# Kernel tuning notes

Measured on AMD Instinct MI355X. Metric: run time of the kernel, lower is better.

The kernel has to match this reference:

```python
import jax, jax.numpy as jnp
import numpy as np

N_NODES = 50000
N_EDGES = 800000
D = 128  # d_feat == hidden_channels


def setup_inputs() -> dict:
    key = jax.random.key(0)
    ks = jax.random.split(key, 7)
    s = 1.0 / np.sqrt(D)
    return {
        "x": jax.random.normal(ks[0], (N_NODES, D), dtype=jnp.float32),
        "edge_index": jax.random.randint(ks[1], (2, N_EDGES), 0, N_NODES, dtype=jnp.int64),
        "W1_l": jax.random.normal(ks[2], (D, D), dtype=jnp.float32) * s,
        "b1": jnp.zeros((D,), dtype=jnp.float32),
        "W1_r": jax.random.normal(ks[3], (D, D), dtype=jnp.float32) * s,
        "W2_l": jax.random.normal(ks[4], (D, D), dtype=jnp.float32) * s,
        "b2": jnp.zeros((D,), dtype=jnp.float32),
        "W2_r": jax.random.normal(ks[5], (D, D), dtype=jnp.float32) * s,
    }


def reference(x, edge_index, W1_l, b1, W1_r, W2_l, b2, W2_r):
    src = edge_index[0]
    dst = edge_index[1]
    n = x.shape[0]
    # in-degree for mean aggregation (zero-degree nodes get 0 aggregate)
    deg = jax.ops.segment_sum(jnp.ones_like(src, dtype=x.dtype), dst, num_segments=n)
    inv_deg = (1.0 / jnp.maximum(deg, 1.0))[:, None]  # [N,1]

    def sage_conv(h, Wl, b, Wr):
        # mean over incoming neighbor messages, then lin_l(agg) + lin_r(h)
        agg = jax.ops.segment_sum(h[src], dst, num_segments=n) * inv_deg  # [N,D]
        return agg @ Wl + b + h @ Wr

    h = jax.nn.relu(sage_conv(x, W1_l, b1, W1_r))
    return sage_conv(h, W2_l, b2, W2_r)
```

## Files before the change

kernel.cpp:

```cpp
#include <hip/hip_runtime.h>
#include <hip/hip_bf16.h>

typedef __attribute__((ext_vector_type(8))) short bf16x8;
typedef __attribute__((ext_vector_type(4))) float f32x4;

#define CAP 64
#define SH  8

static __device__ inline unsigned short f2b(float f) {
    unsigned u = __float_as_uint(f);
    unsigned r = (u + 0x7FFFu + ((u >> 16) & 1u)) >> 16;
    return (unsigned short)r;
}
static __device__ inline float blo(unsigned u) { return __uint_as_float(u << 16); }
static __device__ inline float bhi(unsigned u) { return __uint_as_float(u & 0xFFFF0000u); }

__global__ void zero_kernel(int* __restrict__ p, int n) {
    int i = blockIdx.x * blockDim.x + threadIdx.x;
    if (i < n) p[i] = 0;
}

__global__ __launch_bounds__(256) void fill_shard_kernel(
        const int* __restrict__ ei, int* __restrict__ cursor,
        unsigned short* __restrict__ edge16, int E, int N, int G, int npg) {
    int s = blockIdx.x & (SH - 1);
    int i = blockIdx.x >> 3;
    int d_lo = s * npg;
    int d_hi = d_lo + npg; if (d_hi > N) d_hi = N;
    int C = (E + G - 1) / G;
    int e0 = i * C;
    int e1 = e0 + C; if (e1 > E) e1 = E;
    for (int e = e0 + threadIdx.x; e < e1; e += 256) {
        int d = ei[E + e];
        if (d < d_lo || d >= d_hi) continue;
        int src = ei[e];
        if ((unsigned)src >= (unsigned)N) src = 0;
        int pos = atomicAdd(&cursor[d], 1);
        if (pos < CAP) edge16[(size_t)d * CAP + pos] = (unsigned short)src;
    }
}

__global__ __launch_bounds__(256) void x2b_kernel(const float* __restrict__ x,
                                                  unsigned short* __restrict__ xb,
                                                  int n4) {
    int i = blockIdx.x * blockDim.x + threadIdx.x;
    if (i >= n4) return;
    float4 v = ((const float4*)x)[i];
    ushort4 b;
    b.x = f2b(v.x); b.y = f2b(v.y); b.z = f2b(v.z); b.w = f2b(v.w);
    ((ushort4*)xb)[i] = b;
}

__global__ __launch_bounds__(256) void aggregate_kernel(
        const unsigned short* __restrict__ in, const int* __restrict__ cursor,
        const unsigned short* __restrict__ edge16, const int* __restrict__ ei,
        unsigned short* __restrict__ agg, int E, int N) {
    int node = blockIdx.x * 4 + (threadIdx.x >> 6);
    if (node >= N) return;
    int lane = threadIdx.x & 63;
    int g = lane >> 4;
    int f = lane & 15;
    int deg = cursor[node];

    float acc[8];
    #pragma unroll
    for (int i = 0; i < 8; ++i) acc[i] = 0.f;

    if (deg <= CAP) {
        const unsigned short* base = edge16 + (size_t)node * CAP;
        int idx = (lane < deg) ? (int)base[lane] : 0;
        #pragma unroll 4
        for (int j = 0; j < deg; j += 4) {
            int e = j + g;
            int s = __shfl(idx, e & 63);
            if (e < deg) {
                uint4 v = *(const uint4*)(in + (size_t)s * 128 + f * 8);
                acc[0] += blo(v.x); acc[1] += bhi(v.x);
                acc[2] += blo(v.y); acc[3] += bhi(v.y);
                acc[4] += blo(v.z); acc[5] += bhi(v.z);
                acc[6] += blo(v.w); acc[7] += bhi(v.w);
            }
        }
    } else {
        for (int j = 0; j < E; j += 4) {
            int e = j + g;
            bool act = (e < E) && (ei[E + e] == node);
            if (act) {
                int s = ei[e];
                if ((unsigned)s >= (unsigned)N) s = 0;
                uint4 v = *(const uint4*)(in + (size_t)s * 128 + f * 8);
                acc[0] += blo(v.x); acc[1] += bhi(v.x);
                acc[2] += blo(v.y); acc[3] += bhi(v.y);
                acc[4] += blo(v.z); acc[5] += bhi(v.z);
                acc[6] += blo(v.w); acc[7] += bhi(v.w);
            }
        }
    }

    #pragma unroll
    for (int d = 16; d <= 32; d <<= 1) {
        #pragma unroll
        for (int i = 0; i < 8; ++i) acc[i] += __shfl_xor(acc[i], d);
    }

    if (g == 0) {
        float inv = 1.0f / (float)(deg > 1 ? deg : 1);
        uint4 o;
        o.x = (unsigned)f2b(acc[0] * inv) | ((unsigned)f2b(acc[1] * inv) << 16);
        o.y = (unsigned)f2b(acc[2] * inv) | ((unsigned)f2b(acc[3] * inv) << 16);
        o.z = (unsigned)f2b(acc[4] * inv) | ((unsigned)f2b(acc[5] * inv) << 16);
        o.w = (unsigned)f2b(acc[6] * inv) | ((unsigned)f2b(acc[7] * inv) << 16);
        *(uint4*)(agg + (size_t)node * 128 + f * 8) = o;
    }
}

__global__ void prep_w_kernel(const float* __restrict__ W1l, const float* __restrict__ W1r,
                              const float* __restrict__ W2l, const float* __restrict__ W2r,
                              unsigned short* __restrict__ wt) {
    int n = blockIdx.x & 127;
    int layer = blockIdx.x >> 7;
    int k = threadIdx.x;
    const float* Wlp = layer ? W2l : W1l;
    const float* Wrp = layer ? W2r : W1r;
    unsigned short* dst = wt + (size_t)layer * 128 * 256 + (size_t)n * 256;
    dst[k]       = f2b(Wlp[(size_t)k * 128 + n]);
    dst[k + 128] = f2b(Wrp[(size_t)k * 128 + n]);
}

template<int RELU, int OUT_BF16>
__global__ __launch_bounds__(256) void gemm_mfma_kernel(
        const unsigned short* __restrict__ Arow, const unsigned short* __restrict__ Xrow,
        const unsigned short* __restrict__ Wt, const float* __restrict__ bias,
        void* __restrict__ outp, int n) {
    constexpr int LDK = 264;
    __shared__ unsigned short sA[64 * LDK];
    int tid = threadIdx.x;
    int row0 = blockIdx.x * 64;

    #pragma unroll
    for (int it = 0; it < 8; ++it) {
        int c = tid + it * 256;
        int r = c >> 5;
        int q = c & 31;
        int row = row0 + r; if (row >= n) row = n - 1;
        uint4 v = (q < 16) ? ((const uint4*)(Arow + (size_t)row * 128))[q]
                           : ((const uint4*)(Xrow + (size_t)row * 128))[q - 16];
        *(uint4*)&sA[r * LDK + q * 8] = v;
    }
    __syncthreads();

    int lane = tid & 63;
    int wave = tid >> 6;
    int quad = lane >> 4;
    int tm   = lane & 15;

    f32x4 acc[4][2];
    #pragma unroll
    for (int m = 0; m < 4; ++m)
        #pragma unroll
        for (int j = 0; j < 2; ++j)
            acc[m][j] = (f32x4){0.f, 0.f, 0.f, 0.f};

    const unsigned short* wb0 = Wt + (size_t)(wave * 32 + tm) * 256;

    #pragma unroll
    for (int ks = 0; ks < 8; ++ks) {
        int k0 = ks * 32 + quad * 8;
        bf16x8 a[4], b[2];
        #pragma unroll
        for (int m = 0; m < 4; ++m)
            a[m] = *(const bf16x8*)&sA[(m * 16 + tm) * LDK + k0];
        #pragma unroll
        for (int j = 0; j < 2; ++j)
            b[j] = *(const bf16x8*)(wb0 + (size_t)j * 16 * 256 + k0);
        #pragma unroll
        for (int m = 0; m < 4; ++m)
            #pragma unroll
            for (int j = 0; j < 2; ++j)
                acc[m][j] = __builtin_amdgcn_mfma_f32_16x16x32_bf16(a[m], b[j], acc[m][j], 0, 0, 0);
    }

    #pragma unroll
    for (int j = 0; j < 2; ++j) {
        int ncol = wave * 32 + j * 16 + tm;
        float bb = bias[ncol];
        #pragma unroll
        for (int m = 0; m < 4; ++m) {
            #pragma unroll
            for (int reg = 0; reg < 4; ++reg) {
                int row = row0 + m * 16 + quad * 4 + reg;
                if (row >= n) continue;
                float v = acc[m][j][reg] + bb;
                if (RELU) v = v > 0.f ? v : 0.f;
                if (OUT_BF16)
                    ((unsigned short*)outp)[(size_t)row * 128 + ncol] = f2b(v);
                else
                    ((float*)outp)[(size_t)row * 128 + ncol] = v;
            }
        }
    }
}

extern "C" void kernel_launch(void* const* d_in, const int* in_sizes, int n_in,
                              void* d_out, int out_size, void* d_ws, size_t ws_size,
                              hipStream_t stream) {
    const float* x   = (const float*)d_in[0];
    const int*   ei  = (const int*)d_in[1];
    const float* W1l = (const float*)d_in[2];
    const float* b1  = (const float*)d_in[3];
    const float* W1r = (const float*)d_in[4];
    const float* W2l = (const float*)d_in[5];
    const float* b2  = (const float*)d_in[6];
    const float* W2r = (const float*)d_in[7];
    float* out = (float*)d_out;

    const int D = 128;
    const int N = in_sizes[0] / D;
    const int E = in_sizes[1] / 2;

    char* ws = (char*)d_ws;
    size_t off = 0;
    auto alloc = [&](size_t bytes) {
        size_t o = off;
        off = (off + bytes + 511) & ~(size_t)511;
        return (void*)(ws + o);
    };
    int*            cursor  = (int*)           alloc((size_t)N * 4);
    unsigned short* edge16  = (unsigned short*)alloc((size_t)N * CAP * 2);
    unsigned short* agg_bf  = (unsigned short*)alloc((size_t)N * D * 2);
    unsigned short* xb      = (unsigned short*)alloc((size_t)N * D * 2);
    unsigned short* wt      = (unsigned short*)alloc((size_t)2 * 128 * 256 * 2);
    unsigned short* h_bf = xb;
    (void)ws_size; (void)n_in; (void)out_size;

    zero_kernel<<<(N + 255) / 256, 256, 0, stream>>>(cursor, N);
    {
        int G = 256;
        int npg = (N + SH - 1) / SH;
        fill_shard_kernel<<<SH * G, 256, 0, stream>>>(ei, cursor, edge16, E, N, G, npg);
    }

    int n4 = N * D / 4;
    x2b_kernel<<<(n4 + 255) / 256, 256, 0, stream>>>(x, xb, n4);
    prep_w_kernel<<<256, 128, 0, stream>>>(W1l, W1r, W2l, W2r, wt);
    const unsigned short* wt1 = wt;
    const unsigned short* wt2 = wt + (size_t)128 * 256;

    int agg_grid  = (N + 3) / 4;
    int gemm_grid = (N + 63) / 64;

    aggregate_kernel<<<agg_grid, 256, 0, stream>>>(xb, cursor, edge16, ei, agg_bf, E, N);
    gemm_mfma_kernel<1, 1><<<gemm_grid, 256, 0, stream>>>(agg_bf, xb, wt1, b1, (void*)h_bf, N);

    aggregate_kernel<<<agg_grid, 256, 0, stream>>>(h_bf, cursor, edge16, ei, agg_bf, E, N);
    gemm_mfma_kernel<0, 0><<<gemm_grid, 256, 0, stream>>>(agg_bf, h_bf, wt2, b2, (void*)out, N);
}
```

Baseline: 229.8 us.

## Fuse neighbor aggregation into the MFMA GEMM kernel per layer

```diff
diff --git a/kernel.cpp b/kernel.cpp
--- a/kernel.cpp
+++ b/kernel.cpp
@@ -51,69 +51,6 @@
     ((ushort4*)xb)[i] = b;
 }
 
-__global__ __launch_bounds__(256) void aggregate_kernel(
-        const unsigned short* __restrict__ in, const int* __restrict__ cursor,
-        const unsigned short* __restrict__ edge16, const int* __restrict__ ei,
-        unsigned short* __restrict__ agg, int E, int N) {
-    int node = blockIdx.x * 4 + (threadIdx.x >> 6);
-    if (node >= N) return;
-    int lane = threadIdx.x & 63;
-    int g = lane >> 4;
-    int f = lane & 15;
-    int deg = cursor[node];
-
-    float acc[8];
-    #pragma unroll
-    for (int i = 0; i < 8; ++i) acc[i] = 0.f;
-
-    if (deg <= CAP) {
-        const unsigned short* base = edge16 + (size_t)node * CAP;
-        int idx = (lane < deg) ? (int)base[lane] : 0;
-        #pragma unroll 4
-        for (int j = 0; j < deg; j += 4) {
-            int e = j + g;
-            int s = __shfl(idx, e & 63);
-            if (e < deg) {
-                uint4 v = *(const uint4*)(in + (size_t)s * 128 + f * 8);
-                acc[0] += blo(v.x); acc[1] += bhi(v.x);
-                acc[2] += blo(v.y); acc[3] += bhi(v.y);
-                acc[4] += blo(v.z); acc[5] += bhi(v.z);
-                acc[6] += blo(v.w); acc[7] += bhi(v.w);
-            }
-        }
-    } else {
-        for (int j = 0; j < E; j += 4) {
-            int e = j + g;
-            bool act = (e < E) && (ei[E + e] == node);
-            if (act) {
-                int s = ei[e];
-                if ((unsigned)s >= (unsigned)N) s = 0;
-                uint4 v = *(const uint4*)(in + (size_t)s * 128 + f * 8);
-                acc[0] += blo(v.x); acc[1] += bhi(v.x);
-                acc[2] += blo(v.y); acc[3] += bhi(v.y);
-                acc[4] += blo(v.z); acc[5] += bhi(v.z);
-                acc[6] += blo(v.w); acc[7] += bhi(v.w);
-            }
-        }
-    }
-
-    #pragma unroll
-    for (int d = 16; d <= 32; d <<= 1) {
-        #pragma unroll
-        for (int i = 0; i < 8; ++i) acc[i] += __shfl_xor(acc[i], d);
-    }
-
-    if (g == 0) {
-        float inv = 1.0f / (float)(deg > 1 ? deg : 1);
-        uint4 o;
-        o.x = (unsigned)f2b(acc[0] * inv) | ((unsigned)f2b(acc[1] * inv) << 16);
-        o.y = (unsigned)f2b(acc[2] * inv) | ((unsigned)f2b(acc[3] * inv) << 16);
-        o.z = (unsigned)f2b(acc[4] * inv) | ((unsigned)f2b(acc[5] * inv) << 16);
-        o.w = (unsigned)f2b(acc[6] * inv) | ((unsigned)f2b(acc[7] * inv) << 16);
-        *(uint4*)(agg + (size_t)node * 128 + f * 8) = o;
-    }
-}
-
 __global__ void prep_w_kernel(const float* __restrict__ W1l, const float* __restrict__ W1r,
                               const float* __restrict__ W2l, const float* __restrict__ W2r,
                               unsigned short* __restrict__ wt) {
@@ -128,29 +65,85 @@
 }
 
 template<int RELU, int OUT_BF16>
-__global__ __launch_bounds__(256) void gemm_mfma_kernel(
-        const unsigned short* __restrict__ Arow, const unsigned short* __restrict__ Xrow,
+__global__ __launch_bounds__(256) void layer_kernel(
+        const unsigned short* __restrict__ in, const int* __restrict__ cursor,
+        const unsigned short* __restrict__ edge16, const int* __restrict__ ei,
         const unsigned short* __restrict__ Wt, const float* __restrict__ bias,
-        void* __restrict__ outp, int n) {
+        void* __restrict__ outp, int E, int N) {
     constexpr int LDK = 264;
     __shared__ unsigned short sA[64 * LDK];
-    int tid = threadIdx.x;
-    int row0 = blockIdx.x * 64;
-
-    #pragma unroll
-    for (int it = 0; it < 8; ++it) {
-        int c = tid + it * 256;
-        int r = c >> 5;
-        int q = c & 31;
-        int row = row0 + r; if (row >= n) row = n - 1;
-        uint4 v = (q < 16) ? ((const uint4*)(Arow + (size_t)row * 128))[q]
-                           : ((const uint4*)(Xrow + (size_t)row * 128))[q - 16];
-        *(uint4*)&sA[r * LDK + q * 8] = v;
-    }
-    __syncthreads();
-
+    int tid  = threadIdx.x;
     int lane = tid & 63;
     int wave = tid >> 6;
+    int row0 = blockIdx.x * 64;
+
+    #pragma unroll
+    for (int it = 0; it < 4; ++it) {
+        int c = tid + it * 256;
+        int r = c >> 4;
+        int q = c & 15;
+        int row = row0 + r; if (row >= N) row = N - 1;
+        uint4 v = ((const uint4*)(in + (size_t)row * 128))[q];
+        *(uint4*)&sA[r * LDK + 128 + q * 8] = v;
+    }
+
+    int g = lane >> 4;
+    int f = lane & 15;
+    for (int i = 0; i < 16; ++i) {
+        int node = row0 + wave * 16 + i;
+        if (node >= N) break;
+        int deg = cursor[node];
+        float acc[8];
+        #pragma unroll
+        for (int t = 0; t < 8; ++t) acc[t] = 0.f;
+
+        if (deg <= CAP) {
+            const unsigned short* base = edge16 + (size_t)node * CAP;
+            int idx = (lane < deg) ? (int)base[lane] : 0;
+            #pragma unroll 4
+            for (int j = 0; j < deg; j += 4) {
+                int e = j + g;
+                int s = __shfl(idx, e & 63);
+                if (e < deg) {
+                    uint4 v = *(const uint4*)(in + (size_t)s * 128 + f * 8);
+                    acc[0] += blo(v.x); acc[1] += bhi(v.x);
+                    acc[2] += blo(v.y); acc[3] += bhi(v.y);
+                    acc[4] += blo(v.z); acc[5] += bhi(v.z);
+                    acc[6] += blo(v.w); acc[7] += bhi(v.w);
+                }
+            }
+        } else {
+            for (int j = 0; j < E; j += 4) {
+                int e = j + g;
+                bool act = (e < E) && (ei[E + e] == node);
+                if (act) {
+                    int s = ei[e];
+                    if ((unsigned)s >= (unsigned)N) s = 0;
+                    uint4 v = *(const uint4*)(in + (size_t)s * 128 + f * 8);
+                    acc[0] += blo(v.x); acc[1] += bhi(v.x);
+                    acc[2] += blo(v.y); acc[3] += bhi(v.y);
+                    acc[4] += blo(v.z); acc[5] += bhi(v.z);
+                    acc[6] += blo(v.w); acc[7] += bhi(v.w);
+                }
+            }
+        }
+        #pragma unroll
+        for (int d = 16; d <= 32; d <<= 1) {
+            #pragma unroll
+            for (int t = 0; t < 8; ++t) acc[t] += __shfl_xor(acc[t], d);
+        }
+        if (g == 0) {
+            float inv = 1.0f / (float)(deg > 1 ? deg : 1);
+            uint4 o;
+            o.x = (unsigned)f2b(acc[0] * inv) | ((unsigned)f2b(acc[1] * inv) << 16);
+            o.y = (unsigned)f2b(acc[2] * inv) | ((unsigned)f2b(acc[3] * inv) << 16);
+            o.z = (unsigned)f2b(acc[4] * inv) | ((unsigned)f2b(acc[5] * inv) << 16);
+            o.w = (unsigned)f2b(acc[6] * inv) | ((unsigned)f2b(acc[7] * inv) << 16);
+            *(uint4*)&sA[(wave * 16 + i) * LDK + f * 8] = o;
+        }
+    }
+    __syncthreads();
+
     int quad = lane >> 4;
     int tm   = lane & 15;
 
@@ -189,7 +182,7 @@
             #pragma unroll
             for (int reg = 0; reg < 4; ++reg) {
                 int row = row0 + m * 16 + quad * 4 + reg;
-                if (row >= n) continue;
+                if (row >= N) continue;
                 float v = acc[m][j][reg] + bb;
                 if (RELU) v = v > 0.f ? v : 0.f;
                 if (OUT_BF16)
@@ -227,10 +220,9 @@
     };
     int*            cursor  = (int*)           alloc((size_t)N * 4);
     unsigned short* edge16  = (unsigned short*)alloc((size_t)N * CAP * 2);
-    unsigned short* agg_bf  = (unsigned short*)alloc((size_t)N * D * 2);
     unsigned short* xb      = (unsigned short*)alloc((size_t)N * D * 2);
+    unsigned short* h_bf    = (unsigned short*)alloc((size_t)N * D * 2);
     unsigned short* wt      = (unsigned short*)alloc((size_t)2 * 128 * 256 * 2);
-    unsigned short* h_bf = xb;
     (void)ws_size; (void)n_in; (void)out_size;
 
     zero_kernel<<<(N + 255) / 256, 256, 0, stream>>>(cursor, N);
@@ -246,12 +238,8 @@
     const unsigned short* wt1 = wt;
     const unsigned short* wt2 = wt + (size_t)128 * 256;
 
-    int agg_grid  = (N + 3) / 4;
-    int gemm_grid = (N + 63) / 64;
-
-    aggregate_kernel<<<agg_grid, 256, 0, stream>>>(xb, cursor, edge16, ei, agg_bf, E, N);
-    gemm_mfma_kernel<1, 1><<<gemm_grid, 256, 0, stream>>>(agg_bf, xb, wt1, b1, (void*)h_bf, N);
-
-    aggregate_kernel<<<agg_grid, 256, 0, stream>>>(h_bf, cursor, edge16, ei, agg_bf, E, N);
-    gemm_mfma_kernel<0, 0><<<gemm_grid, 256, 0, stream>>>(agg_bf, h_bf, wt2, b2, (void*)out, N);
-}
+    int grid = (N + 63) / 64;
+
+    layer_kernel<1, 1><<<grid, 256, 0, stream>>>(xb,   cursor, edge16, ei, wt1, b1, (void*)h_bf, E, N);
+    layer_kernel<0, 0><<<grid, 256, 0, stream>>>(h_bf, cursor, edge16, ei, wt2, b2, (void*)out,  E, N);
+}
```

Measured after the change: 260.4 us. 13.3% more time.

## Gather neighbor features in FP8 for mean aggregation, merge conversion kernels

Applied to the files above, without the earlier changes.

```diff
diff --git a/kernel.cpp b/kernel.cpp
--- a/kernel.cpp
+++ b/kernel.cpp
@@ -14,6 +14,11 @@
 }
 static __device__ inline float blo(unsigned u) { return __uint_as_float(u << 16); }
 static __device__ inline float bhi(unsigned u) { return __uint_as_float(u & 0xFFFF0000u); }
+static __device__ inline unsigned pk_fp8x4(float a, float b, float c, float d) {
+    int v = __builtin_amdgcn_cvt_pk_fp8_f32(a, b, 0, false);
+    v = __builtin_amdgcn_cvt_pk_fp8_f32(c, d, v, true);
+    return (unsigned)v;
+}
 
 __global__ void zero_kernel(int* __restrict__ p, int n) {
     int i = blockIdx.x * blockDim.x + threadIdx.x;
@@ -40,91 +45,121 @@
     }
 }
 
-__global__ __launch_bounds__(256) void x2b_kernel(const float* __restrict__ x,
-                                                  unsigned short* __restrict__ xb,
-                                                  int n4) {
+__global__ __launch_bounds__(256) void convert_kernel(
+        const float* __restrict__ x, unsigned short* __restrict__ xb,
+        unsigned char* __restrict__ xf8, int n4,
+        const float* __restrict__ W1l, const float* __restrict__ W1r,
+        const float* __restrict__ W2l, const float* __restrict__ W2r,
+        unsigned short* __restrict__ wt, int G1) {
+    int b = blockIdx.x;
+    if (b < G1) {
+        int i = b * 256 + threadIdx.x;
+        if (i >= n4) return;
+        float4 v = ((const float4*)x)[i];
+        ushort4 o;
+        o.x = f2b(v.x); o.y = f2b(v.y); o.z = f2b(v.z); o.w = f2b(v.w);
+        ((ushort4*)xb)[i] = o;
+        ((unsigned*)xf8)[i] = pk_fp8x4(v.x, v.y, v.z, v.w);
+    } else {
+        int id = (b - G1) * 256 + threadIdx.x;
+        int layer = id >> 15;
+        int rem = id & 32767;
+        int n = rem >> 8;
+        int kk = rem & 255;
+        const float* Wlp = layer ? W2l : W1l;
+        const float* Wrp = layer ? W2r : W1r;
+        float v = (kk < 128) ? Wlp[(size_t)kk * 128 + n]
+                             : Wrp[(size_t)(kk - 128) * 128 + n];
+        wt[(size_t)layer * 32768 + (size_t)n * 256 + kk] = f2b(v);
+    }
+}
+
+__global__ __launch_bounds__(256) void b2f8_kernel(
+        const unsigned short* __restrict__ hb, unsigned char* __restrict__ h8, int n8) {
     int i = blockIdx.x * blockDim.x + threadIdx.x;
-    if (i >= n4) return;
-    float4 v = ((const float4*)x)[i];
-    ushort4 b;
-    b.x = f2b(v.x); b.y = f2b(v.y); b.z = f2b(v.z); b.w = f2b(v.w);
-    ((ushort4*)xb)[i] = b;
-}
-
-__global__ __launch_bounds__(256) void aggregate_kernel(
-        const unsigned short* __restrict__ in, const int* __restrict__ cursor,
+    if (i >= n8) return;
+    uint4 v = ((const uint4*)hb)[i];
+    uint2 o;
+    o.x = pk_fp8x4(blo(v.x), bhi(v.x), blo(v.y), bhi(v.y));
+    o.y = pk_fp8x4(blo(v.z), bhi(v.z), blo(v.w), bhi(v.w));
+    ((uint2*)h8)[i] = o;
+}
+
+__global__ __launch_bounds__(256) void aggregate_f8_kernel(
+        const unsigned char* __restrict__ in8, const int* __restrict__ cursor,
         const unsigned short* __restrict__ edge16, const int* __restrict__ ei,
         unsigned short* __restrict__ agg, int E, int N) {
     int node = blockIdx.x * 4 + (threadIdx.x >> 6);
     if (node >= N) return;
     int lane = threadIdx.x & 63;
-    int g = lane >> 4;
-    int f = lane & 15;
+    int g = lane >> 3;
+    int f = lane & 7;
     int deg = cursor[node];
 
-    float acc[8];
-    #pragma unroll
-    for (int i = 0; i < 8; ++i) acc[i] = 0.f;
+    float acc[16];
+    #pragma unroll
+    for (int t = 0; t < 16; ++t) acc[t] = 0.f;
 
     if (deg <= CAP) {
         const unsigned short* base = edge16 + (size_t)node * CAP;
         int idx = (lane < deg) ? (int)base[lane] : 0;
-        #pragma unroll 4
-        for (int j = 0; j < deg; j += 4) {
+        #pragma unroll 2
+        for (int j = 0; j < deg; j += 8) {
             int e = j + g;
             int s = __shfl(idx, e & 63);
             if (e < deg) {
-                uint4 v = *(const uint4*)(in + (size_t)s * 128 + f * 8);
-                acc[0] += blo(v.x); acc[1] += bhi(v.x);
-                acc[2] += blo(v.y); acc[3] += bhi(v.y);
-                acc[4] += blo(v.z); acc[5] += bhi(v.z);
-                acc[6] += blo(v.w); acc[7] += bhi(v.w);
+                uint4 v = *(const uint4*)(in8 + (size_t)s * 128 + f * 16);
+                #pragma unroll
+                for (int w = 0; w < 4; ++w) {
+                    unsigned dw = (&v.x)[w];
+                    acc[w * 4 + 0] += __builtin_amdgcn_cvt_f32_fp8(dw, 0);
+                    acc[w * 4 + 1] += __builtin_amdgcn_cvt_f32_fp8(dw, 1);
+                    acc[w * 4 + 2] += __builtin_amdgcn_cvt_f32_fp8(dw, 2);
+                    acc[w * 4 + 3] += __builtin_amdgcn_cvt_f32_fp8(dw, 3);
+                }
             }
         }
     } else {
-        for (int j = 0; j < E; j += 4) {
+        for (int j = 0; j < E; j += 8) {
             int e = j + g;
             bool act = (e < E) && (ei[E + e] == node);
             if (act) {
                 int s = ei[e];
                 if ((unsigned)s >= (unsigned)N) s = 0;
-                uint4 v = *(const uint4*)(in + (size_t)s * 128 + f * 8);
-                acc[0] += blo(v.x); acc[1] += bhi(v.x);
-                acc[2] += blo(v.y); acc[3] += bhi(v.y);
-                acc[4] += blo(v.z); acc[5] += bhi(v.z);
-                acc[6] += blo(v.w); acc[7] += bhi(v.w);
+                uint4 v = *(const uint4*)(in8 + (size_t)s * 128 + f * 16);
+                #pragma unroll
+                for (int w = 0; w < 4; ++w) {
+                    unsigned dw = (&v.x)[w];
+                    acc[w * 4 + 0] += __builtin_amdgcn_cvt_f32_fp8(dw, 0);
+                    acc[w * 4 + 1] += __builtin_amdgcn_cvt_f32_fp8(dw, 1);
+                    acc[w * 4 + 2] += __builtin_amdgcn_cvt_f32_fp8(dw, 2);
+                    acc[w * 4 + 3] += __builtin_amdgcn_cvt_f32_fp8(dw, 3);
+                }
             }
         }
     }
 
     #pragma unroll
-    for (int d = 16; d <= 32; d <<= 1) {
-        #pragma unroll
-        for (int i = 0; i < 8; ++i) acc[i] += __shfl_xor(acc[i], d);
+    for (int d = 8; d <= 32; d <<= 1) {
+        #pragma unroll
+        for (int t = 0; t < 16; ++t) acc[t] += __shfl_xor(acc[t], d);
     }
 
     if (g == 0) {
         float inv = 1.0f / (float)(deg > 1 ? deg : 1);
-        uint4 o;
-        o.x = (unsigned)f2b(acc[0] * inv) | ((unsigned)f2b(acc[1] * inv) << 16);
-        o.y = (unsigned)f2b(acc[2] * inv) | ((unsigned)f2b(acc[3] * inv) << 16);
-        o.z = (unsigned)f2b(acc[4] * inv) | ((unsigned)f2b(acc[5] * inv) << 16);
-        o.w = (unsigned)f2b(acc[6] * inv) | ((unsigned)f2b(acc[7] * inv) << 16);
-        *(uint4*)(agg + (size_t)node * 128 + f * 8) = o;
-    }
-}
-
-__global__ void prep_w_kernel(const float* __restrict__ W1l, const float* __restrict__ W1r,
-                              const float* __restrict__ W2l, const float* __restrict__ W2r,
-                              unsigned short* __restrict__ wt) {
-    int n = blockIdx.x & 127;
-    int layer = blockIdx.x >> 7;
-    int k = threadIdx.x;
-    const float* Wlp = layer ? W2l : W1l;
-    const float* Wrp = layer ? W2r : W1r;
-    unsigned short* dst = wt + (size_t)layer * 128 * 256 + (size_t)n * 256;
-    dst[k]       = f2b(Wlp[(size_t)k * 128 + n]);
-    dst[k + 128] = f2b(Wrp[(size_t)k * 128 + n]);
+        uint4 o0, o1;
+        o0.x = (unsigned)f2b(acc[0] * inv)  | ((unsigned)f2b(acc[1] * inv)  << 16);
+        o0.y = (unsigned)f2b(acc[2] * inv)  | ((unsigned)f2b(acc[3] * inv)  << 16);
+        o0.z = (unsigned)f2b(acc[4] * inv)  | ((unsigned)f2b(acc[5] * inv)  << 16);
+        o0.w = (unsigned)f2b(acc[6] * inv)  | ((unsigned)f2b(acc[7] * inv)  << 16);
+        o1.x = (unsigned)f2b(acc[8] * inv)  | ((unsigned)f2b(acc[9] * inv)  << 16);
+        o1.y = (unsigned)f2b(acc[10] * inv) | ((unsigned)f2b(acc[11] * inv) << 16);
+        o1.z = (unsigned)f2b(acc[12] * inv) | ((unsigned)f2b(acc[13] * inv) << 16);
+        o1.w = (unsigned)f2b(acc[14] * inv) | ((unsigned)f2b(acc[15] * inv) << 16);
+        unsigned short* dst = agg + (size_t)node * 128 + f * 16;
+        *(uint4*)dst = o0;
+        *(uint4*)(dst + 8) = o1;
+    }
 }
 
 template<int RELU, int OUT_BF16>
@@ -229,8 +264,10 @@
     unsigned short* edge16  = (unsigned short*)alloc((size_t)N * CAP * 2);
     unsigned short* agg_bf  = (unsigned short*)alloc((size_t)N * D * 2);
     unsigned short* xb      = (unsigned short*)alloc((size_t)N * D * 2);
+    unsigned char*  xf8     = (unsigned char*) alloc((size_t)N * D);
     unsigned short* wt      = (unsigned short*)alloc((size_t)2 * 128 * 256 * 2);
     unsigned short* h_bf = xb;
+    unsigned char*  h_f8 = xf8;
     (void)ws_size; (void)n_in; (void)out_size;
 
     zero_kernel<<<(N + 255) / 256, 256, 0, stream>>>(cursor, N);
@@ -241,17 +278,19 @@
     }
 
     int n4 = N * D / 4;
-    x2b_kernel<<<(n4 + 255) / 256, 256, 0, stream>>>(x, xb, n4);
-    prep_w_kernel<<<256, 128, 0, stream>>>(W1l, W1r, W2l, W2r, wt);
+    int G1 = (n4 + 255) / 256;
+    convert_kernel<<<G1 + 256, 256, 0, stream>>>(x, xb, xf8, n4, W1l, W1r, W2l, W2r, wt, G1);
     const unsigned short* wt1 = wt;
     const unsigned short* wt2 = wt + (size_t)128 * 256;
 
     int agg_grid  = (N + 3) / 4;
     int gemm_grid = (N + 63) / 64;
-
-    aggregate_kernel<<<agg_grid, 256, 0, stream>>>(xb, cursor, edge16, ei, agg_bf, E, N);
+    int n8 = N * D / 8;
+
+    aggregate_f8_kernel<<<agg_grid, 256, 0, stream>>>(xf8, cursor, edge16, ei, agg_bf, E, N);
     gemm_mfma_kernel<1, 1><<<gemm_grid, 256, 0, stream>>>(agg_bf, xb, wt1, b1, (void*)h_bf, N);
 
-    aggregate_kernel<<<agg_grid, 256, 0, stream>>>(h_bf, cursor, edge16, ei, agg_bf, E, N);
+    b2f8_kernel<<<(n8 + 255) / 256, 256, 0, stream>>>(h_bf, h_f8, n8);
+    aggregate_f8_kernel<<<agg_grid, 256, 0, stream>>>(h_f8, cursor, edge16, ei, agg_bf, E, N);
     gemm_mfma_kernel<0, 0><<<gemm_grid, 256, 0, stream>>>(agg_bf, h_bf, wt2, b2, (void*)out, N);
 }
```

Measured after the change: 234.9 us. 1.02x slower.
